# Kernel tuning notes

Hardware: AMD Instinct MI355X
Metric: run time of the kernel (lower is better)

Reference implementation:

```python
import jax, jax.numpy as jnp
import numpy as np

B, N, D = 2, 2048, 2048
H = 16
HD = D // H          # 128
R = 512              # kv_rank
INT4_MIN, INT4_MAX = -8, 7


def setup_inputs() -> dict:
    key = jax.random.key(0)
    ks = jax.random.split(key, 6)
    sD = 1.0 / np.sqrt(D)
    sR = 1.0 / np.sqrt(R)
    return {
        "x":   jax.random.normal(ks[0], (B, N, D), dtype=jnp.float32),
        "Wq":  jax.random.normal(ks[1], (D, D), dtype=jnp.float32) * sD,
        "bq":  jnp.zeros((D,), dtype=jnp.float32),
        "Wkv": jax.random.normal(ks[2], (D, R), dtype=jnp.float32) * sD,
        "bkv": jnp.zeros((R,), dtype=jnp.float32),
        "Wku": jax.random.normal(ks[3], (R, D), dtype=jnp.float32) * sR,
        "bku": jnp.zeros((D,), dtype=jnp.float32),
        "Wvu": jax.random.normal(ks[4], (R, D), dtype=jnp.float32) * sR,
        "bvu": jnp.zeros((D,), dtype=jnp.float32),
        "Wo":  jax.random.normal(ks[5], (D, D), dtype=jnp.float32) * sD * 0.1,
        "bo":  jnp.zeros((D,), dtype=jnp.float32),
    }


def _int4_quant_dequant(t):
    # per_channel=True, 3D tensor: amax over dims [0,1], keepdim
    amax = jnp.max(jnp.abs(t), axis=(0, 1), keepdims=True)
    amax = jnp.maximum(amax, 1e-5)
    scale = (amax / 7.0).astype(jnp.float32)
    q = jnp.clip(jnp.round(t / scale), INT4_MIN, INT4_MAX).astype(jnp.int8)
    return q.astype(jnp.float32) * scale


def reference(x, Wq, bq, Wkv, bkv, Wku, bku, Wvu, bvu, Wo, bo):
    q = x @ Wq + bq                              # (B,N,D)
    kv_latent = x @ Wkv + bkv                    # (B,N,R)
    kv_latent = _int4_quant_dequant(kv_latent)   # use_cache=True path
    k = kv_latent @ Wku + bku                    # (B,N,D)
    v = kv_latent @ Wvu + bvu                    # (B,N,D)

    q4 = q.reshape(B, N, H, HD)
    k4 = k.reshape(B, N, H, HD)
    v4 = v.reshape(B, N, H, HD)

    attn = jnp.einsum("bqhd,bkhd->bhqk", q4, k4) * (HD ** -0.5)
    attn = jax.nn.softmax(attn.astype(jnp.float32), axis=-1).astype(x.dtype)
    out = jnp.einsum("bhqk,bkhd->bqhd", attn, v4).reshape(B, N, D)
    return out @ Wo + bo
```

## Files before the change

### kernel.cpp

```cpp
#include <hip/hip_runtime.h>
#include <stdint.h>

typedef __attribute__((ext_vector_type(8))) _Float16 half8;
typedef __attribute__((ext_vector_type(4))) _Float16 half4;
typedef __attribute__((ext_vector_type(4))) float f32x4;

#define AS1 __attribute__((address_space(1)))
#define AS3 __attribute__((address_space(3)))

__device__ inline void gload_lds16(const void* g, void* l) {
  __builtin_amdgcn_global_load_lds((const AS1 void*)g, (AS3 void*)l, 16, 0, 0);
}
__device__ inline f32x4 mfma16h(half8 a, half8 b, f32x4 c) {
  return __builtin_amdgcn_mfma_f32_16x16x32_f16(a, b, c, 0, 0, 0);
}

__global__ __launch_bounds__(256) void cvt_split(const float4* __restrict__ in,
                                                 half4* __restrict__ xh,
                                                 half4* __restrict__ xl, int nq) {
  int i = blockIdx.x * 256 + threadIdx.x;
  if (i >= nq) return;
  float4 v = in[i];
  float vv[4] = {v.x, v.y, v.z, v.w};
  half4 h, lo;
#pragma unroll
  for (int j = 0; j < 4; ++j) {
    _Float16 hh = (_Float16)vv[j];
    h[j] = hh;
    lo[j] = (_Float16)((vv[j] - (float)hh) * 4096.0f);
  }
  xh[i] = h;
  xl[i] = lo;
}

__global__ __launch_bounds__(256) void transpose_f16(const float* __restrict__ in,
                                                     _Float16* __restrict__ outh,
                                                     _Float16* __restrict__ outl,
                                                     const float* __restrict__ rowamax,
                                                     int R, int C) {
  __shared__ float t[32][33];
  const int tx = threadIdx.x, ty = threadIdx.y;
  const int r0 = blockIdx.y * 32, c0 = blockIdx.x * 32;
#pragma unroll
  for (int k = 0; k < 4; ++k) {
    const int r = r0 + ty + k * 8;
    float s = 1.0f;
    if (rowamax) s = fmaxf(rowamax[r], 1e-5f) / 7.0f;
    t[ty + k * 8][tx] = in[(size_t)r * C + c0 + tx] * s;
  }
  __syncthreads();
#pragma unroll
  for (int k = 0; k < 4; ++k) {
    const int c = c0 + ty + k * 8;
    float v = t[tx][ty + k * 8];
    _Float16 h = (_Float16)v;
    outh[(size_t)c * R + r0 + tx] = h;
    if (outl) outl[(size_t)c * R + r0 + tx] = (_Float16)((v - (float)h) * 4096.0f);
  }
}

__global__ __launch_bounds__(256) void gemm_kv16(const _Float16* __restrict__ Ah,
                                                 const _Float16* __restrict__ Al,
                                                 const _Float16* __restrict__ Bh,
                                                 const _Float16* __restrict__ Bl,
                                                 const float* __restrict__ bias,
                                                 float* __restrict__ C,
                                                 float* __restrict__ amax,
                                                 int M, int N, int K) {
  __shared__ _Float16 sAh[128 * 64], sAl[128 * 64];
  __shared__ _Float16 sBh[64 * 64], sBl[64 * 64];
  const int tid = threadIdx.x;
  const int w = tid >> 6, l = tid & 63, g = l >> 4, c = l & 15;
  const int wr = w >> 1, wc = w & 1;
  const int tm0 = blockIdx.y * 128, n0 = blockIdx.x * 64;

  f32x4 acc[4][2], acc2[4][2];
#pragma unroll
  for (int i = 0; i < 4; ++i)
#pragma unroll
    for (int j = 0; j < 2; ++j) {
      acc[i][j] = f32x4{0.f, 0.f, 0.f, 0.f};
      acc2[i][j] = f32x4{0.f, 0.f, 0.f, 0.f};
    }

  for (int k0 = 0; k0 < K; k0 += 64) {
#pragma unroll
    for (int cc = 0; cc < 4; ++cc) {
      const int off = w * 4096 + cc * 1024 + l * 16;
      const int row = off >> 7, colb = off & 127;
      const char* gA = (const char*)Ah + ((size_t)(tm0 + row) * K + k0) * 2 + colb;
      const char* gL = (const char*)Al + ((size_t)(tm0 + row) * K + k0) * 2 + colb;
      gload_lds16(gA, (char*)sAh + w * 4096 + cc * 1024);
      gload_lds16(gL, (char*)sAl + w * 4096 + cc * 1024);
    }
#pragma unroll
    for (int cc = 0; cc < 2; ++cc) {
      const int off = w * 2048 + cc * 1024 + l * 16;
      const int row = off >> 7, colb = off & 127;
      const char* gB = (const char*)Bh + ((size_t)(n0 + row) * K + k0) * 2 + colb;
      const char* gL = (const char*)Bl + ((size_t)(n0 + row) * K + k0) * 2 + colb;
      gload_lds16(gB, (char*)sBh + w * 2048 + cc * 1024);
      gload_lds16(gL, (char*)sBl + w * 2048 + cc * 1024);
    }
    __syncthreads();
#pragma unroll
    for (int ks = 0; ks < 2; ++ks) {
      half8 ah[4], al[4], bh[2], bl[2];
#pragma unroll
      for (int i = 0; i < 4; ++i) {
        ah[i] = *(const half8*)&sAh[(wr * 64 + i * 16 + c) * 64 + ks * 32 + g * 8];
        al[i] = *(const half8*)&sAl[(wr * 64 + i * 16 + c) * 64 + ks * 32 + g * 8];
      }
#pragma unroll
      for (int j = 0; j < 2; ++j) {
        bh[j] = *(const half8*)&sBh[(wc * 32 + j * 16 + c) * 64 + ks * 32 + g * 8];
        bl[j] = *(const half8*)&sBl[(wc * 32 + j * 16 + c) * 64 + ks * 32 + g * 8];
      }
#pragma unroll
      for (int i = 0; i < 4; ++i)
#pragma unroll
        for (int j = 0; j < 2; ++j) {
          acc[i][j] = mfma16h(ah[i], bh[j], acc[i][j]);
          acc2[i][j] = mfma16h(al[i], bh[j], acc2[i][j]);
          acc2[i][j] = mfma16h(ah[i], bl[j], acc2[i][j]);
        }
    }
    __syncthreads();
  }

  float cm[2] = {0.f, 0.f};
#pragma unroll
  for (int i = 0; i < 4; ++i) {
    const int row0 = tm0 + wr * 64 + i * 16 + g * 4;
#pragma unroll
    for (int j = 0; j < 2; ++j) {
      const int col = n0 + wc * 32 + j * 16 + c;
      const float bv = bias[col];
#pragma unroll
      for (int r = 0; r < 4; ++r) {
        float v = acc[i][j][r] + acc2[i][j][r] * 2.44140625e-4f + bv;
        C[(size_t)(row0 + r) * N + col] = v;
        cm[j] = fmaxf(cm[j], fabsf(v));
      }
    }
  }
#pragma unroll
  for (int j = 0; j < 2; ++j) {
    float m = cm[j];
    m = fmaxf(m, __shfl_xor(m, 16, 64));
    m = fmaxf(m, __shfl_xor(m, 32, 64));
    if (g == 0) atomicMax((int*)amax + (n0 + wc * 32 + j * 16 + c), __float_as_int(m));
  }
}

__global__ __launch_bounds__(256) void quant_kernel(const float4* __restrict__ kv,
                                                    const float* __restrict__ amax,
                                                    half4* __restrict__ kvq, int nq) {
  int i = blockIdx.x * 256 + threadIdx.x;
  if (i >= nq) return;
  float4 v = kv[i];
  int r0 = (i * 4) & 511;
  half4 o;
#pragma unroll
  for (int j = 0; j < 4; ++j) {
    float s = fmaxf(amax[r0 + j], 1e-5f) / 7.0f;
    float val = (j == 0) ? v.x : (j == 1) ? v.y : (j == 2) ? v.z : v.w;
    float q = rintf(val / s);
    q = fminf(7.f, fmaxf(-8.f, q));
    o[j] = (_Float16)q;
  }
  kvq[i] = o;
}

template <int MODE>
__global__ __launch_bounds__(256) void gemm_bt(const _Float16* __restrict__ A,
                                               const _Float16* __restrict__ BT,
                                               void* __restrict__ Cout,
                                               const float* __restrict__ bias,
                                               int M, int N, int K) {
  __shared__ _Float16 As[128 * 64];
  __shared__ _Float16 Bs[128 * 64];
  const int tid = threadIdx.x;
  const int w = tid >> 6, l = tid & 63, g = l >> 4, c = l & 15;
  const int wr = w >> 1, wc = w & 1;
  const int tm0 = blockIdx.y * 128, tn0 = blockIdx.x * 128;

  f32x4 acc[4][4];
#pragma unroll
  for (int i = 0; i < 4; ++i)
#pragma unroll
    for (int j = 0; j < 4; ++j) acc[i][j] = f32x4{0.f, 0.f, 0.f, 0.f};

  for (int k0 = 0; k0 < K; k0 += 64) {
#pragma unroll
    for (int cc = 0; cc < 4; ++cc) {
      const int off = w * 4096 + cc * 1024 + l * 16;
      const int row = off >> 7, colb = off & 127;
      const char* gA = (const char*)A + ((size_t)(tm0 + row) * K + k0) * 2 + colb;
      const char* gB = (const char*)BT + ((size_t)(tn0 + row) * K + k0) * 2 + colb;
      gload_lds16(gA, (char*)As + w * 4096 + cc * 1024);
      gload_lds16(gB, (char*)Bs + w * 4096 + cc * 1024);
    }
    __syncthreads();
#pragma unroll
    for (int ks = 0; ks < 2; ++ks) {
      half8 a[4], b[4];
#pragma unroll
      for (int i = 0; i < 4; ++i)
        a[i] = *(const half8*)&As[(wr * 64 + i * 16 + c) * 64 + ks * 32 + g * 8];
#pragma unroll
      for (int j = 0; j < 4; ++j)
        b[j] = *(const half8*)&Bs[(wc * 64 + j * 16 + c) * 64 + ks * 32 + g * 8];
#pragma unroll
      for (int i = 0; i < 4; ++i)
#pragma unroll
        for (int j = 0; j < 4; ++j) acc[i][j] = mfma16h(a[i], b[j], acc[i][j]);
    }
    __syncthreads();
  }

#pragma unroll
  for (int i = 0; i < 4; ++i) {
    const int row0 = tm0 + wr * 64 + i * 16 + g * 4;
#pragma unroll
    for (int j = 0; j < 4; ++j) {
      const int col = tn0 + wc * 64 + j * 16 + c;
      const float bv = bias[col];
      if constexpr (MODE == 0) {
#pragma unroll
        for (int r = 0; r < 4; ++r)
          ((_Float16*)Cout)[(size_t)(row0 + r) * N + col] = (_Float16)(acc[i][j][r] + bv);
      } else if constexpr (MODE == 1) {
        half4 pk;
#pragma unroll
        for (int r = 0; r < 4; ++r) pk[r] = (_Float16)(acc[i][j][r] + bv);
        const int bI = row0 >> 11, nI = row0 & 2047, hI = col >> 7, dI = col & 127;
        *(half4*)((_Float16*)Cout +
                  (size_t)((bI * 16 + hI) * 32 + (nI >> 6)) * 8192 + dI * 64 + (nI & 63)) = pk;
      } else if constexpr (MODE == 3) {
        const int bI = row0 >> 11, hI = col >> 7, dI = col & 127;
#pragma unroll
        for (int r = 0; r < 4; ++r) {
          const int n = (row0 + r) & 2047;
          ((_Float16*)Cout)[(size_t)((bI * 16 + hI) * 32 + (n >> 6)) * 8192 +
                            (n & 63) * 128 + dI] = (_Float16)(acc[i][j][r] + bv);
        }
      } else {
#pragma unroll
        for (int r = 0; r < 4; ++r)
          ((float*)Cout)[(size_t)(row0 + r) * N + col] = acc[i][j][r] + bv;
      }
    }
  }
}

#define SCALE_QK 0.08838834764831845f
__global__ __launch_bounds__(256, 2) void flash_attn(const _Float16* __restrict__ Q,
                                                     const _Float16* __restrict__ KB,
                                                     const _Float16* __restrict__ VB,
                                                     _Float16* __restrict__ O) {
  __shared__ _Float16 Ks[2][8192];
  __shared__ _Float16 Vs[2][8192];
  __shared__ _Float16 Ps[4][2048];
  const int tid = threadIdx.x, w = tid >> 6, l = tid & 63, g = l >> 4, c = l & 15;
  const int wgid = blockIdx.x + blockIdx.y * 16;
  const int xcd = wgid & 7, idx = wgid >> 3;
  const int bh = xcd * 4 + (idx >> 4), qblk = idx & 15;
  const int b = bh >> 4, h = bh & 15;
  const size_t rowQ0 = (size_t)b * 2048 + qblk * 128 + w * 32;
  const _Float16* kvK = KB + (size_t)bh * 262144;
  const _Float16* kvV = VB + (size_t)bh * 262144;
  const int sxc = (c & 7) ^ ((c >> 1) & 6);

  auto stageK = [&](int t, int buf) {
#pragma unroll
    for (int i = 0; i < 4; ++i) {
      const int o = i * 4096 + w * 1024 + l * 16;
      const int row = o >> 8;
      const int src = (o & ~255) | ((o & 255) ^ ((row & 7) << 4));
      gload_lds16((const char*)(kvK + t * 8192) + src,
                  (char*)&Ks[buf][0] + i * 4096 + w * 1024);
    }
  };
  auto stageV = [&](int t, int buf) {
#pragma unroll
    for (int i = 0; i < 4; ++i) {
      const int o = i * 4096 + w * 1024 + l * 16;
      const int row = o >> 7;
      const int src = (o & ~127) | ((o & 127) ^ ((row & 7) << 4));
      gload_lds16((const char*)(kvV + t * 8192) + src,
                  (char*)&Vs[buf][0] + i * 4096 + w * 1024);
    }
  };

  stageK(0, 0);
  stageV(0, 0);
  half8 aq[2][4];
#pragma unroll
  for (int m = 0; m < 2; ++m)
#pragma unroll
    for (int ks = 0; ks < 4; ++ks)
      aq[m][ks] = *(const half8*)&Q[(rowQ0 + m * 16 + c) * 2048 + h * 128 + ks * 32 + g * 8];

  f32x4 accO[2][8];
#pragma unroll
  for (int m = 0; m < 2; ++m)
#pragma unroll
    for (int n = 0; n < 8; ++n) accO[m][n] = f32x4{0.f, 0.f, 0.f, 0.f};
  float lsum[2][4];
#pragma unroll
  for (int m = 0; m < 2; ++m)
#pragma unroll
    for (int r = 0; r < 4; ++r) lsum[m][r] = 0.f;

  __syncthreads();

  for (int t = 0; t < 32; ++t) {
    const int cur = t & 1;
    if (t < 31) { stageK(t + 1, cur ^ 1); stageV(t + 1, cur ^ 1); }
    f32x4 accS[2][4];
#pragma unroll
    for (int m = 0; m < 2; ++m)
#pragma unroll
      for (int n = 0; n < 4; ++n) accS[m][n] = f32x4{0.f, 0.f, 0.f, 0.f};
    __builtin_amdgcn_s_setprio(1);
#pragma unroll
    for (int ks = 0; ks < 4; ++ks) {
      half8 bk[4];
#pragma unroll
      for (int n = 0; n < 4; ++n) {
        const int row = n * 16 + c;
        bk[n] = *(const half8*)((const char*)&Ks[cur][0] + row * 256 +
                                ((ks * 64 + g * 16) ^ ((c & 7) << 4)));
      }
#pragma unroll
      for (int m = 0; m < 2; ++m)
#pragma unroll
        for (int n = 0; n < 4; ++n) accS[m][n] = mfma16h(aq[m][ks], bk[n], accS[m][n]);
    }
    __builtin_amdgcn_s_setprio(0);
#pragma unroll
    for (int m = 0; m < 2; ++m)
#pragma unroll
      for (int n = 0; n < 4; ++n)
#pragma unroll
        for (int r = 0; r < 4; ++r) {
          const float p = __expf(accS[m][n][r] * SCALE_QK);
          lsum[m][r] += p;
          const int row = m * 16 + g * 4 + r;
          const int sxw = ((row & 7) ^ ((row >> 1) & 6));
          *(_Float16*)((char*)&Ps[w][0] + row * 128 +
                       ((n * 32 + c * 2) ^ (sxw << 4))) = (_Float16)p;
        }
    __builtin_amdgcn_s_setprio(1);
#pragma unroll
    for (int ks = 0; ks < 2; ++ks) {
      half8 ap[2];
#pragma unroll
      for (int m = 0; m < 2; ++m) {
        const int row = m * 16 + c;
        ap[m] = *(const half8*)((const char*)&Ps[w][0] + row * 128 +
                                ((ks * 64 + g * 16) ^ (sxc << 4)));
      }
#pragma unroll
      for (int n = 0; n < 8; ++n) {
        const int vrow = n * 16 + c;
        half8 bv = *(const half8*)((const char*)&Vs[cur][0] + vrow * 128 +
                                   ((ks * 64 + g * 16) ^ ((c & 7) << 4)));
#pragma unroll
        for (int m = 0; m < 2; ++m) accO[m][n] = mfma16h(ap[m], bv, accO[m][n]);
      }
    }
    __builtin_amdgcn_s_setprio(0);
    __syncthreads();
  }

#pragma unroll
  for (int m = 0; m < 2; ++m)
#pragma unroll
    for (int r = 0; r < 4; ++r) {
      float ps = lsum[m][r];
#pragma unroll
      for (int off = 1; off < 16; off <<= 1) ps += __shfl_xor(ps, off, 64);
      const float inv = 1.f / ps;
#pragma unroll
      for (int n = 0; n < 8; ++n) {
        float v = accO[m][n][r] * inv;
        O[(rowQ0 + m * 16 + g * 4 + r) * 2048 + h * 128 + n * 16 + c] = (_Float16)v;
      }
    }
}

extern "C" void kernel_launch(void* const* d_in, const int* in_sizes, int n_in,
                              void* d_out, int out_size, void* d_ws, size_t ws_size,
                              hipStream_t stream) {
  const float* x   = (const float*)d_in[0];
  const float* Wq  = (const float*)d_in[1];
  const float* bq  = (const float*)d_in[2];
  const float* Wkv = (const float*)d_in[3];
  const float* bkv = (const float*)d_in[4];
  const float* Wku = (const float*)d_in[5];
  const float* bku = (const float*)d_in[6];
  const float* Wvu = (const float*)d_in[7];
  const float* bvu = (const float*)d_in[8];
  const float* Wo  = (const float*)d_in[9];
  const float* bo  = (const float*)d_in[10];
  float* out = (float*)d_out;

  char* ws = (char*)d_ws;
  const size_t MB = 1ull << 20;
  _Float16* xh   = (_Float16*)(ws + 0 * MB);
  _Float16* attn = (_Float16*)(ws + 0 * MB);
  _Float16* xl   = (_Float16*)(ws + 16 * MB);
  _Float16* qb   = (_Float16*)(ws + 16 * MB);
  _Float16* kb   = (_Float16*)(ws + 32 * MB);
  _Float16* vT   = (_Float16*)(ws + 48 * MB);
  _Float16* WqT  = (_Float16*)(ws + 64 * MB);
  _Float16* WoT  = (_Float16*)(ws + 72 * MB);
  float* kv      = (float*)(ws + 80 * MB);
  _Float16* kvq  = (_Float16*)(ws + 88 * MB);
  _Float16* WkvTh = (_Float16*)(ws + 92 * MB);
  _Float16* WkvTl = (_Float16*)(ws + 94 * MB);
  _Float16* WkuT = (_Float16*)(ws + 96 * MB);
  _Float16* WvuT = (_Float16*)(ws + 98 * MB);
  float* amax    = (float*)(ws + 100 * MB);

  hipMemsetAsync(amax, 0, 512 * sizeof(float), stream);

  cvt_split<<<8192, 256, 0, stream>>>((const float4*)x, (half4*)xh, (half4*)xl, 2097152);
  transpose_f16<<<dim3(64, 64), dim3(32, 8), 0, stream>>>(Wq, WqT, nullptr, nullptr, 2048, 2048);
  transpose_f16<<<dim3(16, 64), dim3(32, 8), 0, stream>>>(Wkv, WkvTh, WkvTl, nullptr, 2048, 512);
  transpose_f16<<<dim3(64, 64), dim3(32, 8), 0, stream>>>(Wo, WoT, nullptr, nullptr, 2048, 2048);
  gemm_kv16<<<dim3(8, 32), 256, 0, stream>>>(xh, xl, WkvTh, WkvTl, bkv, kv, amax, 4096, 512, 2048);
  quant_kernel<<<2048, 256, 0, stream>>>((const float4*)kv, amax, (half4*)kvq, 524288);
  transpose_f16<<<dim3(64, 16), dim3(32, 8), 0, stream>>>(Wku, WkuT, nullptr, amax, 512, 2048);
  transpose_f16<<<dim3(64, 16), dim3(32, 8), 0, stream>>>(Wvu, WvuT, nullptr, amax, 512, 2048);
  gemm_bt<0><<<dim3(16, 32), 256, 0, stream>>>(xh, WqT, qb, bq, 4096, 2048, 2048);
  gemm_bt<3><<<dim3(16, 32), 256, 0, stream>>>(kvq, WkuT, kb, bku, 4096, 2048, 512);
  gemm_bt<1><<<dim3(16, 32), 256, 0, stream>>>(kvq, WvuT, vT, bvu, 4096, 2048, 512);
  flash_attn<<<dim3(16, 32), 256, 0, stream>>>(qb, kb, vT, attn);
  gemm_bt<2><<<dim3(16, 32), 256, 0, stream>>>(attn, WoT, out, bo, 4096, 2048, 2048);

  (void)in_sizes; (void)n_in; (void)out_size; (void)ws_size;
}
```

Baseline: 336.4 us.

## Batch weight transposes, fuse K/V up-projections, fold QK scale, widen attention blocks

Merges the Wq/Wo and Wku/Wvu transposes into single launches via a z grid dimension, and fuses the K and V up-projection GEMMs into one GEMM with N=4096 that writes both layouts. The softmax scale is folded into the Q projection epilogue, which removes a multiply from the attention inner loop. Flash attention now runs with 512 threads per block, 8 waves each owning 16 query rows instead of 4 waves with 32, and launch bounds ask for more resident blocks. This trades per-wave reuse of K/V fragments for more waves to hide latency, and relies on WkuT and WvuT being contiguous in the workspace.

Result: no change. 337.9 us (+0.4%).

```diff
diff --git a/kernel.cpp b/kernel.cpp
--- a/kernel.cpp
+++ b/kernel.cpp
@@ -34,11 +34,13 @@
 }
 
 __global__ __launch_bounds__(256) void transpose_f16(const float* __restrict__ in,
+                                                     const float* __restrict__ in2,
                                                      _Float16* __restrict__ outh,
                                                      _Float16* __restrict__ outl,
                                                      const float* __restrict__ rowamax,
                                                      int R, int C) {
   __shared__ float t[32][33];
+  if (blockIdx.z) { in = in2; outh += (size_t)R * C; }
   const int tx = threadIdx.x, ty = threadIdx.y;
   const int r0 = blockIdx.y * 32, c0 = blockIdx.x * 32;
 #pragma unroll
@@ -176,7 +178,10 @@
 __global__ __launch_bounds__(256) void gemm_bt(const _Float16* __restrict__ A,
                                                const _Float16* __restrict__ BT,
                                                void* __restrict__ Cout,
+                                               void* __restrict__ Cout2,
                                                const float* __restrict__ bias,
+                                               const float* __restrict__ bias2,
+                                               float cscale,
                                                int M, int N, int K) {
   __shared__ _Float16 As[128 * 64];
   __shared__ _Float16 Bs[128 * 64];
@@ -225,27 +230,35 @@
 #pragma unroll
     for (int j = 0; j < 4; ++j) {
       const int col = tn0 + wc * 64 + j * 16 + c;
-      const float bv = bias[col];
       if constexpr (MODE == 0) {
+        const float bv = bias[col];
 #pragma unroll
         for (int r = 0; r < 4; ++r)
-          ((_Float16*)Cout)[(size_t)(row0 + r) * N + col] = (_Float16)(acc[i][j][r] + bv);
-      } else if constexpr (MODE == 1) {
-        half4 pk;
-#pragma unroll
-        for (int r = 0; r < 4; ++r) pk[r] = (_Float16)(acc[i][j][r] + bv);
-        const int bI = row0 >> 11, nI = row0 & 2047, hI = col >> 7, dI = col & 127;
-        *(half4*)((_Float16*)Cout +
-                  (size_t)((bI * 16 + hI) * 32 + (nI >> 6)) * 8192 + dI * 64 + (nI & 63)) = pk;
-      } else if constexpr (MODE == 3) {
-        const int bI = row0 >> 11, hI = col >> 7, dI = col & 127;
-#pragma unroll
-        for (int r = 0; r < 4; ++r) {
-          const int n = (row0 + r) & 2047;
-          ((_Float16*)Cout)[(size_t)((bI * 16 + hI) * 32 + (n >> 6)) * 8192 +
-                            (n & 63) * 128 + dI] = (_Float16)(acc[i][j][r] + bv);
+          ((_Float16*)Cout)[(size_t)(row0 + r) * N + col] =
+              (_Float16)((acc[i][j][r] + bv) * cscale);
+      } else if constexpr (MODE == 4) {
+        const int bI = row0 >> 11;
+        const int colk = col & 2047;
+        const int hI = colk >> 7, dI = colk & 127;
+        if (col < 2048) {
+          const float bv = bias[colk];
+#pragma unroll
+          for (int r = 0; r < 4; ++r) {
+            const int n = (row0 + r) & 2047;
+            ((_Float16*)Cout)[(size_t)((bI * 16 + hI) * 32 + (n >> 6)) * 8192 +
+                              (n & 63) * 128 + dI] = (_Float16)(acc[i][j][r] + bv);
+          }
+        } else {
+          const float bv = bias2[colk];
+          half4 pk;
+#pragma unroll
+          for (int r = 0; r < 4; ++r) pk[r] = (_Float16)(acc[i][j][r] + bv);
+          const int nI = row0 & 2047;
+          *(half4*)((_Float16*)Cout2 +
+                    (size_t)((bI * 16 + hI) * 32 + (nI >> 6)) * 8192 + dI * 64 + (nI & 63)) = pk;
         }
       } else {
+        const float bv = bias[col];
 #pragma unroll
         for (int r = 0; r < 4; ++r)
           ((float*)Cout)[(size_t)(row0 + r) * N + col] = acc[i][j][r] + bv;
@@ -254,75 +267,64 @@
   }
 }
 
-#define SCALE_QK 0.08838834764831845f
-__global__ __launch_bounds__(256, 2) void flash_attn(const _Float16* __restrict__ Q,
+__global__ __launch_bounds__(512, 4) void flash_attn(const _Float16* __restrict__ Q,
                                                      const _Float16* __restrict__ KB,
                                                      const _Float16* __restrict__ VB,
                                                      _Float16* __restrict__ O) {
   __shared__ _Float16 Ks[2][8192];
   __shared__ _Float16 Vs[2][8192];
-  __shared__ _Float16 Ps[4][2048];
+  __shared__ _Float16 Ps[8][1024];
   const int tid = threadIdx.x, w = tid >> 6, l = tid & 63, g = l >> 4, c = l & 15;
   const int wgid = blockIdx.x + blockIdx.y * 16;
   const int xcd = wgid & 7, idx = wgid >> 3;
   const int bh = xcd * 4 + (idx >> 4), qblk = idx & 15;
   const int b = bh >> 4, h = bh & 15;
-  const size_t rowQ0 = (size_t)b * 2048 + qblk * 128 + w * 32;
+  const size_t rowQ0 = (size_t)b * 2048 + qblk * 128 + w * 16;
   const _Float16* kvK = KB + (size_t)bh * 262144;
   const _Float16* kvV = VB + (size_t)bh * 262144;
   const int sxc = (c & 7) ^ ((c >> 1) & 6);
 
   auto stageK = [&](int t, int buf) {
 #pragma unroll
-    for (int i = 0; i < 4; ++i) {
-      const int o = i * 4096 + w * 1024 + l * 16;
+    for (int i = 0; i < 2; ++i) {
+      const int o = i * 8192 + tid * 16;
       const int row = o >> 8;
       const int src = (o & ~255) | ((o & 255) ^ ((row & 7) << 4));
       gload_lds16((const char*)(kvK + t * 8192) + src,
-                  (char*)&Ks[buf][0] + i * 4096 + w * 1024);
+                  (char*)&Ks[buf][0] + i * 8192 + w * 1024);
     }
   };
   auto stageV = [&](int t, int buf) {
 #pragma unroll
-    for (int i = 0; i < 4; ++i) {
-      const int o = i * 4096 + w * 1024 + l * 16;
+    for (int i = 0; i < 2; ++i) {
+      const int o = i * 8192 + tid * 16;
       const int row = o >> 7;
       const int src = (o & ~127) | ((o & 127) ^ ((row & 7) << 4));
       gload_lds16((const char*)(kvV + t * 8192) + src,
-                  (char*)&Vs[buf][0] + i * 4096 + w * 1024);
+                  (char*)&Vs[buf][0] + i * 8192 + w * 1024);
     }
   };
 
   stageK(0, 0);
   stageV(0, 0);
-  half8 aq[2][4];
-#pragma unroll
-  for (int m = 0; m < 2; ++m)
-#pragma unroll
-    for (int ks = 0; ks < 4; ++ks)
-      aq[m][ks] = *(const half8*)&Q[(rowQ0 + m * 16 + c) * 2048 + h * 128 + ks * 32 + g * 8];
-
-  f32x4 accO[2][8];
-#pragma unroll
-  for (int m = 0; m < 2; ++m)
-#pragma unroll
-    for (int n = 0; n < 8; ++n) accO[m][n] = f32x4{0.f, 0.f, 0.f, 0.f};
-  float lsum[2][4];
-#pragma unroll
-  for (int m = 0; m < 2; ++m)
-#pragma unroll
-    for (int r = 0; r < 4; ++r) lsum[m][r] = 0.f;
+  half8 aq[4];
+#pragma unroll
+  for (int ks = 0; ks < 4; ++ks)
+    aq[ks] = *(const half8*)&Q[(rowQ0 + c) * 2048 + h * 128 + ks * 32 + g * 8];
+
+  f32x4 accO[8];
+#pragma unroll
+  for (int n = 0; n < 8; ++n) accO[n] = f32x4{0.f, 0.f, 0.f, 0.f};
+  float lsum[4] = {0.f, 0.f, 0.f, 0.f};
 
   __syncthreads();
 
   for (int t = 0; t < 32; ++t) {
     const int cur = t & 1;
     if (t < 31) { stageK(t + 1, cur ^ 1); stageV(t + 1, cur ^ 1); }
-    f32x4 accS[2][4];
-#pragma unroll
-    for (int m = 0; m < 2; ++m)
-#pragma unroll
-      for (int n = 0; n < 4; ++n) accS[m][n] = f32x4{0.f, 0.f, 0.f, 0.f};
+    f32x4 accS[4];
+#pragma unroll
+    for (int n = 0; n < 4; ++n) accS[n] = f32x4{0.f, 0.f, 0.f, 0.f};
     __builtin_amdgcn_s_setprio(1);
 #pragma unroll
     for (int ks = 0; ks < 4; ++ks) {
@@ -334,41 +336,31 @@
                                 ((ks * 64 + g * 16) ^ ((c & 7) << 4)));
       }
 #pragma unroll
-      for (int m = 0; m < 2; ++m)
-#pragma unroll
-        for (int n = 0; n < 4; ++n) accS[m][n] = mfma16h(aq[m][ks], bk[n], accS[m][n]);
+      for (int n = 0; n < 4; ++n) accS[n] = mfma16h(aq[ks], bk[n], accS[n]);
     }
     __builtin_amdgcn_s_setprio(0);
 #pragma unroll
-    for (int m = 0; m < 2; ++m)
-#pragma unroll
-      for (int n = 0; n < 4; ++n)
-#pragma unroll
-        for (int r = 0; r < 4; ++r) {
-          const float p = __expf(accS[m][n][r] * SCALE_QK);
-          lsum[m][r] += p;
-          const int row = m * 16 + g * 4 + r;
-          const int sxw = ((row & 7) ^ ((row >> 1) & 6));
-          *(_Float16*)((char*)&Ps[w][0] + row * 128 +
-                       ((n * 32 + c * 2) ^ (sxw << 4))) = (_Float16)p;
-        }
+    for (int n = 0; n < 4; ++n)
+#pragma unroll
+      for (int r = 0; r < 4; ++r) {
+        const float p = __expf(accS[n][r]);
+        lsum[r] += p;
+        const int row = g * 4 + r;
+        const int sxw = ((row & 7) ^ ((row >> 1) & 6));
+        *(_Float16*)((char*)&Ps[w][0] + row * 128 +
+                     ((n * 32 + c * 2) ^ (sxw << 4))) = (_Float16)p;
+      }
     __builtin_amdgcn_s_setprio(1);
 #pragma unroll
     for (int ks = 0; ks < 2; ++ks) {
-      half8 ap[2];
-#pragma unroll
-      for (int m = 0; m < 2; ++m) {
-        const int row = m * 16 + c;
-        ap[m] = *(const half8*)((const char*)&Ps[w][0] + row * 128 +
-                                ((ks * 64 + g * 16) ^ (sxc << 4)));
-      }
+      half8 ap = *(const half8*)((const char*)&Ps[w][0] + c * 128 +
+                                 ((ks * 64 + g * 16) ^ (sxc << 4)));
 #pragma unroll
       for (int n = 0; n < 8; ++n) {
         const int vrow = n * 16 + c;
         half8 bv = *(const half8*)((const char*)&Vs[cur][0] + vrow * 128 +
                                    ((ks * 64 + g * 16) ^ ((c & 7) << 4)));
-#pragma unroll
-        for (int m = 0; m < 2; ++m) accO[m][n] = mfma16h(ap[m], bv, accO[m][n]);
+        accO[n] = mfma16h(ap, bv, accO[n]);
       }
     }
     __builtin_amdgcn_s_setprio(0);
@@ -376,20 +368,20 @@
   }
 
 #pragma unroll
-  for (int m = 0; m < 2; ++m)
-#pragma unroll
-    for (int r = 0; r < 4; ++r) {
-      float ps = lsum[m][r];
-#pragma unroll
-      for (int off = 1; off < 16; off <<= 1) ps += __shfl_xor(ps, off, 64);
-      const float inv = 1.f / ps;
-#pragma unroll
-      for (int n = 0; n < 8; ++n) {
-        float v = accO[m][n][r] * inv;
-        O[(rowQ0 + m * 16 + g * 4 + r) * 2048 + h * 128 + n * 16 + c] = (_Float16)v;
-      }
-    }
-}
+  for (int r = 0; r < 4; ++r) {
+    float ps = lsum[r];
+#pragma unroll
+    for (int off = 1; off < 16; off <<= 1) ps += __shfl_xor(ps, off, 64);
+    const float inv = 1.f / ps;
+#pragma unroll
+    for (int n = 0; n < 8; ++n) {
+      float v = accO[n][r] * inv;
+      O[(rowQ0 + g * 4 + r) * 2048 + h * 128 + n * 16 + c] = (_Float16)v;
+    }
+  }
+}
+
+#define SCALE_QK 0.08838834764831845f
 
 extern "C" void kernel_launch(void* const* d_in, const int* in_sizes, int n_in,
                               void* d_out, int out_size, void* d_ws, size_t ws_size,
@@ -428,18 +420,18 @@
   hipMemsetAsync(amax, 0, 512 * sizeof(float), stream);
 
   cvt_split<<<8192, 256, 0, stream>>>((const float4*)x, (half4*)xh, (half4*)xl, 2097152);
-  transpose_f16<<<dim3(64, 64), dim3(32, 8), 0, stream>>>(Wq, WqT, nullptr, nullptr, 2048, 2048);
-  transpose_f16<<<dim3(16, 64), dim3(32, 8), 0, stream>>>(Wkv, WkvTh, WkvTl, nullptr, 2048, 512);
-  transpose_f16<<<dim3(64, 64), dim3(32, 8), 0, stream>>>(Wo, WoT, nullptr, nullptr, 2048, 2048);
+  transpose_f16<<<dim3(64, 64, 2), dim3(32, 8), 0, stream>>>(Wq, Wo, WqT, nullptr, nullptr, 2048, 2048);
+  transpose_f16<<<dim3(16, 64), dim3(32, 8), 0, stream>>>(Wkv, nullptr, WkvTh, WkvTl, nullptr, 2048, 512);
   gemm_kv16<<<dim3(8, 32), 256, 0, stream>>>(xh, xl, WkvTh, WkvTl, bkv, kv, amax, 4096, 512, 2048);
   quant_kernel<<<2048, 256, 0, stream>>>((const float4*)kv, amax, (half4*)kvq, 524288);
-  transpose_f16<<<dim3(64, 16), dim3(32, 8), 0, stream>>>(Wku, WkuT, nullptr, amax, 512, 2048);
-  transpose_f16<<<dim3(64, 16), dim3(32, 8), 0, stream>>>(Wvu, WvuT, nullptr, amax, 512, 2048);
-  gemm_bt<0><<<dim3(16, 32), 256, 0, stream>>>(xh, WqT, qb, bq, 4096, 2048, 2048);
-  gemm_bt<3><<<dim3(16, 32), 256, 0, stream>>>(kvq, WkuT, kb, bku, 4096, 2048, 512);
-  gemm_bt<1><<<dim3(16, 32), 256, 0, stream>>>(kvq, WvuT, vT, bvu, 4096, 2048, 512);
-  flash_attn<<<dim3(16, 32), 256, 0, stream>>>(qb, kb, vT, attn);
-  gemm_bt<2><<<dim3(16, 32), 256, 0, stream>>>(attn, WoT, out, bo, 4096, 2048, 2048);
+  transpose_f16<<<dim3(64, 16, 2), dim3(32, 8), 0, stream>>>(Wku, Wvu, WkuT, nullptr, amax, 512, 2048);
+  gemm_bt<0><<<dim3(16, 32), 256, 0, stream>>>(xh, WqT, qb, nullptr, bq, nullptr, SCALE_QK,
+                                               4096, 2048, 2048);
+  gemm_bt<4><<<dim3(32, 32), 256, 0, stream>>>(kvq, WkuT, kb, vT, bku, bvu, 1.0f,
+                                               4096, 4096, 512);
+  flash_attn<<<dim3(16, 32), 512, 0, stream>>>(qb, kb, vT, attn);
+  gemm_bt<2><<<dim3(16, 32), 256, 0, stream>>>(attn, WoT, out, nullptr, bo, nullptr, 1.0f,
+                                               4096, 2048, 2048);
 
   (void)in_sizes; (void)n_in; (void)out_size; (void)ws_size;
 }
```
